# Performance work log

Measured on AMD Instinct MI355X. Metric: run time of the kernel, lower is better.

The kernel has to match this reference:

```python
import jax, jax.numpy as jnp
import numpy as np

NUM_HEADS = 4
NUM_GROUPS = 8
EPS = 1e-5


def group_norm(x, gamma, beta):
    # x: [b, c, h, w], GroupNorm with NUM_GROUPS groups, eps=1e-5
    b, c, h, w = x.shape
    xg = x.reshape(b, NUM_GROUPS, (c // NUM_GROUPS) * h * w)
    mean = jnp.mean(xg, axis=-1, keepdims=True)
    var = jnp.var(xg, axis=-1, keepdims=True)
    xn = ((xg - mean) * jax.lax.rsqrt(var + EPS)).reshape(b, c, h, w)
    return xn * gamma[None, :, None, None] + beta[None, :, None, None]


def setup_inputs() -> dict:
    key = jax.random.key(0)
    ks = jax.random.split(key, 4)
    b, c, h, w = 4, 256, 64, 64
    x = jax.random.normal(ks[0], (b, c, h, w), dtype=jnp.float32)
    gamma = jnp.ones((c,), dtype=jnp.float32)
    beta = jnp.zeros((c,), dtype=jnp.float32)
    w_qkv = jax.random.normal(ks[1], (3 * c, c), dtype=jnp.float32) * (c ** -0.5)
    b_qkv = jnp.zeros((3 * c,), dtype=jnp.float32)
    w_proj = jax.random.normal(ks[2], (c, c), dtype=jnp.float32) * (c ** -0.5)
    b_proj = jnp.zeros((c,), dtype=jnp.float32)
    return {"x": x, "gamma": gamma, "beta": beta, "w_qkv": w_qkv,
            "b_qkv": b_qkv, "w_proj": w_proj, "b_proj": b_proj}


def reference(x, gamma, beta, w_qkv, b_qkv, w_proj, b_proj):
    b, c, h, w = x.shape
    heads = NUM_HEADS
    dim = c // heads
    n = h * w
    residual = x
    xn = group_norm(x, gamma, beta)
    # 1x1 conv == per-pixel linear: [b,c,h,w] x [3c,c] -> [b,3c,h,w]
    qkv = jnp.einsum('bchw,oc->bohw', xn, w_qkv) + b_qkv[None, :, None, None]
    # channel layout: (three, heads, dim)
    qkv = qkv.reshape(b, 3, heads, dim, n)            # [b,3,H,D,N]
    qkv = jnp.transpose(qkv, (1, 0, 2, 4, 3))         # [3,b,H,N,D]
    q, k, v = qkv[0], qkv[1], qkv[2]
    scale = dim ** -0.5
    scores = jnp.einsum('bhid,bhjd->bhij', q * scale, k)  # [b,H,N,N]
    attn = jax.nn.softmax(scores, axis=-1)
    out = jnp.einsum('bhij,bhjd->bhid', attn, v)          # [b,H,N,D]
    out = jnp.transpose(out, (0, 1, 3, 2)).reshape(b, c, h, w)
    out = jnp.einsum('bchw,oc->bohw', out, w_proj) + b_proj[None, :, None, None]
    return out + residual
```

## Files before the change

kernel.cpp:

```cpp
#include <hip/hip_runtime.h>
#include <stdint.h>

typedef unsigned short ushort_t;
typedef __attribute__((ext_vector_type(8))) short bf16x8;
typedef __attribute__((ext_vector_type(4))) float f32x4;
typedef __attribute__((ext_vector_type(16))) float f32x16;
typedef __attribute__((ext_vector_type(4))) unsigned int u32x4;

__device__ __forceinline__ ushort_t f2bf(float f) {
  union { float f; unsigned u; } v; v.f = f;
  unsigned r = v.u + 0x7fffu + ((v.u >> 16) & 1u);
  return (ushort_t)(r >> 16);
}
__device__ __forceinline__ unsigned bfbits(float f) {
  union { float f; unsigned u; } v; v.f = f; return v.u;
}
__device__ __forceinline__ unsigned pack_trunc(float lo, float hi) {
#if __has_builtin(__builtin_amdgcn_perm)
  return __builtin_amdgcn_perm(bfbits(hi), bfbits(lo), 0x07060302u);
#else
  return (bfbits(lo) >> 16) | (bfbits(hi) & 0xffff0000u);
#endif
}
__device__ __forceinline__ unsigned pack_rn(float lo, float hi) {
  return (unsigned)f2bf(lo) | ((unsigned)f2bf(hi) << 16);
}
__device__ __forceinline__ void swap32(unsigned &a, unsigned &b) {
#if __has_builtin(__builtin_amdgcn_permlane32_swap)
  auto r = __builtin_amdgcn_permlane32_swap(a, b, false, false);
  a = r[0]; b = r[1];
#else
  asm volatile("v_permlane32_swap_b32 %0, %1" : "+v"(a), "+v"(b));
#endif
}
__device__ __forceinline__ float fast_exp2(float x) {
#if __has_builtin(__builtin_amdgcn_exp2f)
  return __builtin_amdgcn_exp2f(x);
#else
  float r; asm("v_exp_f32 %0, %1" : "=v"(r) : "v"(x)); return r;
#endif
}

#define SCALE_Q 0.18033688011112042f
#define EXP_BIAS 23.083109273961734f

__global__ __launch_bounds__(256)
void gn_stats1(const float* __restrict__ x, float2* __restrict__ partial) {
  int blk = blockIdx.x, tid = threadIdx.x;
  const float* base = x + (size_t)blk * 16384;
  float s = 0.f, ss = 0.f;
  for (int i = tid * 4; i < 16384; i += 1024) {
    float4 v = *(const float4*)(base + i);
    s  += v.x + v.y + v.z + v.w;
    ss += v.x*v.x + v.y*v.y + v.z*v.z + v.w*v.w;
  }
  __shared__ float rs[256], rss[256];
  rs[tid] = s; rss[tid] = ss;
  __syncthreads();
  for (int off = 128; off > 0; off >>= 1) {
    if (tid < off) { rs[tid] += rs[tid+off]; rss[tid] += rss[tid+off]; }
    __syncthreads();
  }
  if (tid == 0) partial[blk] = make_float2(rs[0], rss[0]);
}

__global__ __launch_bounds__(256)
void gn_apply_t(const float* __restrict__ x, const float2* __restrict__ partial,
                const float* __restrict__ gamma, const float* __restrict__ beta,
                ushort_t* __restrict__ xn_t, int b0) {
  int blk = blockIdx.x;
  int tid = threadIdx.x;
  int ct = blk & 7;
  int nt = (blk >> 3) & 15;
  int bl = blk >> 7;
  int b  = b0 + bl;
  int c0 = ct * 32;
  float s = 0.f, ss = 0.f;
  #pragma unroll
  for (int kk = 0; kk < 8; kk++) {
    float2 p = partial[(b*8 + ct)*8 + kk];
    s += p.x; ss += p.y;
  }
  float mean = s * (1.f/131072.f);
  float rstd = rsqrtf(ss * (1.f/131072.f) - mean*mean + 1e-5f);
  __shared__ ushort_t Ls[32][264];
  for (int idx = tid; idx < 32*64; idx += 256) {
    int cc = idx >> 6, seg = idx & 63;
    float ga = gamma[c0+cc], be = beta[c0+cc];
    float a = rstd * ga;
    float bb = be - mean * a;
    float4 v = *(const float4*)(x + ((size_t)(b*256 + c0 + cc))*4096 + nt*256 + seg*4);
    ushort4 t4 = make_ushort4(f2bf(v.x*a+bb), f2bf(v.y*a+bb), f2bf(v.z*a+bb), f2bf(v.w*a+bb));
    *(ushort4*)&Ls[cc][seg*4] = t4;
  }
  __syncthreads();
  for (int idx = tid; idx < 256*4; idx += 256) {
    int n = idx >> 2, seg = idx & 3;
    union { ushort_t u[8]; uint4 v; } pk;
    #pragma unroll
    for (int e = 0; e < 8; e++) pk.u[e] = Ls[seg*8 + e][n];
    *(uint4*)(xn_t + ((size_t)(bl*4096 + nt*256 + n))*256 + c0 + seg*8) = pk.v;
  }
}

__global__ __launch_bounds__(256)
void wconv2(const float* __restrict__ wq, const float* __restrict__ wp,
            ushort_t* __restrict__ oq, ushort_t* __restrict__ op) {
  int blk = blockIdx.x;
  const float* w; ushort_t* o; int i;
  if (blk < 192) { w = wq; o = oq; i = blk*256 + threadIdx.x; }
  else           { w = wp; o = op; i = (blk-192)*256 + threadIdx.x; }
  float4 v = *(const float4*)(w + (size_t)i*4);
  *(ushort4*)(o + (size_t)i*4) = make_ushort4(f2bf(v.x), f2bf(v.y), f2bf(v.z), f2bf(v.w));
}

__global__ __launch_bounds__(256)
void gemm_qkv(const ushort_t* __restrict__ A, const ushort_t* __restrict__ Bt,
              const float* __restrict__ bias, ushort_t* __restrict__ q,
              ushort_t* __restrict__ kbuf, ushort_t* __restrict__ vt,
              int b0, int cpx) {
  int L = blockIdx.x;
  int blk = (L & 7) * cpx + (L >> 3);
  int nt = blk % 12, mt = blk / 12;
  int m0 = mt*128, n0 = nt*64;
  int tid = threadIdx.x;
  int wave = tid >> 6, lane = tid & 63, quad = lane >> 4, l16 = lane & 15;
  __shared__ ushort_t As[128][40];
  __shared__ ushort_t Bs[64][40];
  __shared__ ushort_t Lt[64][136];
  f32x4 acc[2][4];
  #pragma unroll
  for (int i = 0; i < 2; i++)
    #pragma unroll
    for (int j = 0; j < 4; j++) acc[i][j] = (f32x4){0.f,0.f,0.f,0.f};

  for (int k0 = 0; k0 < 256; k0 += 32) {
    #pragma unroll
    for (int i = tid; i < 512; i += 256) {
      int row = i >> 2, seg = i & 3;
      *(uint4*)&As[row][seg*8] = *(const uint4*)(A + (size_t)(m0+row)*256 + k0 + seg*8);
    }
    {
      int row = tid >> 2, seg = tid & 3;
      *(uint4*)&Bs[row][seg*8] = *(const uint4*)(Bt + (size_t)(n0+row)*256 + k0 + seg*8);
    }
    __syncthreads();
    bf16x8 af[2], bfr[4];
    #pragma unroll
    for (int t = 0; t < 2; t++) af[t]  = *(const bf16x8*)&As[wave*32 + t*16 + l16][quad*8];
    #pragma unroll
    for (int t = 0; t < 4; t++) bfr[t] = *(const bf16x8*)&Bs[t*16 + l16][quad*8];
    #pragma unroll
    for (int ti = 0; ti < 2; ti++)
      #pragma unroll
      for (int jn = 0; jn < 4; jn++)
        acc[ti][jn] = __builtin_amdgcn_mfma_f32_16x16x32_bf16(af[ti], bfr[jn], acc[ti][jn], 0, 0, 0);
    __syncthreads();
  }

  int region = nt >> 2;
  if (region == 0) {
    #pragma unroll
    for (int jn = 0; jn < 4; jn++) {
      int n = n0 + jn*16 + l16;
      float bv = bias[n];
      #pragma unroll
      for (int ti = 0; ti < 2; ti++) {
        int mrow = m0 + wave*32 + ti*16 + quad*4;
        #pragma unroll
        for (int r = 0; r < 4; r++)
          q[(size_t)(b0*4096 + mrow + r)*256 + n] = f2bf((acc[ti][jn][r] + bv) * SCALE_Q);
      }
    }
  } else if (region == 1) {
    #pragma unroll
    for (int jn = 0; jn < 4; jn++) {
      int n = n0 + jn*16 + l16;
      float bv = bias[n];
      #pragma unroll
      for (int ti = 0; ti < 2; ti++) {
        int mrow = m0 + wave*32 + ti*16 + quad*4;
        #pragma unroll
        for (int r = 0; r < 4; r++)
          kbuf[(size_t)(b0*4096 + mrow + r)*256 + (n - 256)] = f2bf(acc[ti][jn][r] + bv);
      }
    }
  } else {
    int hh = nt - 8;
    int b_loc = m0 >> 12;
    #pragma unroll
    for (int jn = 0; jn < 4; jn++) {
      int n = n0 + jn*16 + l16;
      float bv = bias[n];
      int drow = jn*16 + l16;
      #pragma unroll
      for (int ti = 0; ti < 2; ti++) {
        int tcol = wave*32 + ti*16 + quad*4;
        uint2 w;
        w.x = pack_rn(acc[ti][jn][0] + bv, acc[ti][jn][1] + bv);
        w.y = pack_rn(acc[ti][jn][2] + bv, acc[ti][jn][3] + bv);
        *(uint2*)&Lt[drow][tcol] = w;
      }
    }
    __syncthreads();
    size_t vb_ = ((size_t)((b0 + b_loc)*4 + hh)*64)*4096 + (size_t)(m0 & 4095);
    for (int idx = tid; idx < 1024; idx += 256) {
      int dd = idx >> 4, toff = (idx & 15)*8;
      *(uint4*)(vt + vb_ + (size_t)dd*4096 + toff) = *(const uint4*)&Lt[dd][toff];
    }
  }
}

__global__ __launch_bounds__(256)
void attn(ushort_t* __restrict__ q, const ushort_t* __restrict__ k,
          const ushort_t* __restrict__ vt, int cpx) {
  int L = blockIdx.x;
  int blk = (L & 7) * cpx + (L >> 3);
  int it = blk & 31;
  int h  = (blk >> 5) & 3;
  int b  = blk >> 7;
  int i0 = it * 128;
  int tid = threadIdx.x;
  int wave = tid >> 6, lane = tid & 63;
  int q32 = lane & 31, hi = lane >> 5;

  __shared__ ushort_t Ks[2][64][72];
  __shared__ ushort_t Vs[2][64][72];

  const ushort_t* kbase = k + (size_t)(b*4096)*256 + h*64;
  const ushort_t* vbase = vt + (size_t)(b*4 + h)*64*4096;
  ushort_t* qrow = q + (size_t)(b*4096 + i0 + wave*32 + q32)*256 + h*64;

  bf16x8 qb0 = *(const bf16x8*)(qrow      + hi*8);
  bf16x8 qb1 = *(const bf16x8*)(qrow + 16 + hi*8);
  bf16x8 qb2 = *(const bf16x8*)(qrow + 32 + hi*8);
  bf16x8 qb3 = *(const bf16x8*)(qrow + 48 + hi*8);

  bf16x8 ones;
  #pragma unroll
  for (int e = 0; e < 8; e++) ones[e] = (short)0x3F80;

  f32x16 bias_init;
  #pragma unroll
  for (int r = 0; r < 16; r++) bias_init[r] = -EXP_BIAS;

  f32x16 o_acc0, o_acc1, l_acc;
  #pragma unroll
  for (int r = 0; r < 16; r++) { o_acc0[r] = 0.f; o_acc1[r] = 0.f; l_acc[r] = 0.f; }

  int srow = tid >> 2, scol = (tid & 3) * 16;
  const ushort_t* kp = kbase + (size_t)srow*256 + scol;
  const ushort_t* vp = vbase + (size_t)srow*4096 + scol;
  uint4 rk0, rk1, rv0, rv1;
  #define LOADK() { \
    rk0 = *(const uint4*)(kp); \
    rk1 = *(const uint4*)(kp + 8); \
    kp += 64*256; }
  #define WRITEK(BI) { \
    *(uint4*)&Ks[BI][srow][scol]     = rk0; \
    *(uint4*)&Ks[BI][srow][scol + 8] = rk1; }
  #define LOADV() { \
    rv0 = *(const uint4*)(vp); \
    rv1 = *(const uint4*)(vp + 8); \
    vp += 64; }
  #define WRITEV(BI) { \
    *(uint4*)&Vs[BI][srow][scol]     = rv0; \
    *(uint4*)&Vs[BI][srow][scol + 8] = rv1; }

  #define SOFTMAX(S, PB0, PB1) \
    _Pragma("unroll") \
    for (int r = 0; r < 16; r++) S[r] = fast_exp2(S[r]); \
    { unsigned pkA = pack_trunc(S[0],  S[1]),  pkB = pack_trunc(S[2],  S[3]); \
      unsigned pkC = pack_trunc(S[4],  S[5]),  pkD = pack_trunc(S[6],  S[7]); \
      unsigned pkE = pack_trunc(S[8],  S[9]),  pkF = pack_trunc(S[10], S[11]); \
      unsigned pkG = pack_trunc(S[12], S[13]), pkH = pack_trunc(S[14], S[15]); \
      swap32(pkA, pkC); swap32(pkB, pkD); \
      swap32(pkE, pkG); swap32(pkF, pkH); \
      u32x4 w0_ = {pkA, pkB, pkC, pkD}; \
      u32x4 w1_ = {pkE, pkF, pkG, pkH}; \
      PB0 = __builtin_bit_cast(bf16x8, w0_); \
      PB1 = __builtin_bit_cast(bf16x8, w1_); }

  #define WINDOW(BI) { \
    bf16x8 k00 = *(const bf16x8*)&Ks[BI][q32     ][hi*8]; \
    bf16x8 k01 = *(const bf16x8*)&Ks[BI][q32     ][16 + hi*8]; \
    bf16x8 k02 = *(const bf16x8*)&Ks[BI][q32     ][32 + hi*8]; \
    bf16x8 k03 = *(const bf16x8*)&Ks[BI][q32     ][48 + hi*8]; \
    bf16x8 k10 = *(const bf16x8*)&Ks[BI][32 + q32][hi*8]; \
    bf16x8 k11 = *(const bf16x8*)&Ks[BI][32 + q32][16 + hi*8]; \
    bf16x8 k12 = *(const bf16x8*)&Ks[BI][32 + q32][32 + hi*8]; \
    bf16x8 k13 = *(const bf16x8*)&Ks[BI][32 + q32][48 + hi*8]; \
    bf16x8 va00 = *(const bf16x8*)&Vs[BI][q32     ][hi*8]; \
    bf16x8 va01 = *(const bf16x8*)&Vs[BI][q32     ][16 + hi*8]; \
    bf16x8 va10 = *(const bf16x8*)&Vs[BI][32 + q32][hi*8]; \
    bf16x8 va11 = *(const bf16x8*)&Vs[BI][32 + q32][16 + hi*8]; \
    __builtin_amdgcn_s_setprio(1); \
    f32x16 s0 = __builtin_amdgcn_mfma_f32_32x32x16_bf16(k00, qb0, bias_init, 0, 0, 0); \
    s0 = __builtin_amdgcn_mfma_f32_32x32x16_bf16(k01, qb1, s0, 0, 0, 0); \
    s0 = __builtin_amdgcn_mfma_f32_32x32x16_bf16(k02, qb2, s0, 0, 0, 0); \
    s0 = __builtin_amdgcn_mfma_f32_32x32x16_bf16(k03, qb3, s0, 0, 0, 0); \
    f32x16 s1 = __builtin_amdgcn_mfma_f32_32x32x16_bf16(k10, qb0, bias_init, 0, 0, 0); \
    s1 = __builtin_amdgcn_mfma_f32_32x32x16_bf16(k11, qb1, s1, 0, 0, 0); \
    s1 = __builtin_amdgcn_mfma_f32_32x32x16_bf16(k12, qb2, s1, 0, 0, 0); \
    s1 = __builtin_amdgcn_mfma_f32_32x32x16_bf16(k13, qb3, s1, 0, 0, 0); \
    __builtin_amdgcn_s_setprio(0); \
    bf16x8 vc00 = *(const bf16x8*)&Vs[BI][q32     ][32 + hi*8]; \
    bf16x8 vc01 = *(const bf16x8*)&Vs[BI][q32     ][48 + hi*8]; \
    bf16x8 vc10 = *(const bf16x8*)&Vs[BI][32 + q32][32 + hi*8]; \
    bf16x8 vc11 = *(const bf16x8*)&Vs[BI][32 + q32][48 + hi*8]; \
    bf16x8 pb00, pb01, pb10, pb11; \
    SOFTMAX(s0, pb00, pb01)    \
    __builtin_amdgcn_s_setprio(1); \
    o_acc0 = __builtin_amdgcn_mfma_f32_32x32x16_bf16(va00, pb00, o_acc0, 0, 0, 0); \
    o_acc0 = __builtin_amdgcn_mfma_f32_32x32x16_bf16(va01, pb01, o_acc0, 0, 0, 0); \
    o_acc1 = __builtin_amdgcn_mfma_f32_32x32x16_bf16(va10, pb00, o_acc1, 0, 0, 0); \
    o_acc1 = __builtin_amdgcn_mfma_f32_32x32x16_bf16(va11, pb01, o_acc1, 0, 0, 0); \
    l_acc  = __builtin_amdgcn_mfma_f32_32x32x16_bf16(ones, pb00, l_acc, 0, 0, 0); \
    l_acc  = __builtin_amdgcn_mfma_f32_32x32x16_bf16(ones, pb01, l_acc, 0, 0, 0); \
    __builtin_amdgcn_s_setprio(0); \
    SOFTMAX(s1, pb10, pb11)    \
    __builtin_amdgcn_s_setprio(1); \
    o_acc0 = __builtin_amdgcn_mfma_f32_32x32x16_bf16(vc00, pb10, o_acc0, 0, 0, 0); \
    o_acc0 = __builtin_amdgcn_mfma_f32_32x32x16_bf16(vc01, pb11, o_acc0, 0, 0, 0); \
    o_acc1 = __builtin_amdgcn_mfma_f32_32x32x16_bf16(vc10, pb10, o_acc1, 0, 0, 0); \
    o_acc1 = __builtin_amdgcn_mfma_f32_32x32x16_bf16(vc11, pb11, o_acc1, 0, 0, 0); \
    l_acc  = __builtin_amdgcn_mfma_f32_32x32x16_bf16(ones, pb10, l_acc, 0, 0, 0); \
    l_acc  = __builtin_amdgcn_mfma_f32_32x32x16_bf16(ones, pb11, l_acc, 0, 0, 0); \
    __builtin_amdgcn_s_setprio(0); \
  }

  LOADK(); LOADV(); WRITEK(0); WRITEV(0);
  __syncthreads();

  #pragma unroll 2
  for (int w = 0; w < 64; w++) {
    int cur = w & 1;
    if (w < 63) { LOADK(); LOADV(); }
    WINDOW(cur)
    if (w < 63) { WRITEK(cur ^ 1); WRITEV(cur ^ 1); }
    __syncthreads();
  }
  #undef LOADK
  #undef LOADV
  #undef WRITEK
  #undef WRITEV
  #undef WINDOW
  #undef SOFTMAX

  float inv = 1.f / l_acc[0];

  #pragma unroll
  for (int g = 0; g < 4; g++) {
    ushort4 u;
    u.x = f2bf(o_acc0[g*4+0]*inv); u.y = f2bf(o_acc0[g*4+1]*inv);
    u.z = f2bf(o_acc0[g*4+2]*inv); u.w = f2bf(o_acc0[g*4+3]*inv);
    *(ushort4*)(qrow + g*8 + hi*4) = u;
  }
  #pragma unroll
  for (int g = 0; g < 4; g++) {
    ushort4 u;
    u.x = f2bf(o_acc1[g*4+0]*inv); u.y = f2bf(o_acc1[g*4+1]*inv);
    u.z = f2bf(o_acc1[g*4+2]*inv); u.w = f2bf(o_acc1[g*4+3]*inv);
    *(ushort4*)(qrow + 32 + g*8 + hi*4) = u;
  }
}

__global__ __launch_bounds__(256)
void gemm_proj(const ushort_t* __restrict__ A,
               const ushort_t* __restrict__ Bt,
               const float* __restrict__ bias, const float* __restrict__ resid,
               float* __restrict__ out, int col_base) {
  int blk = blockIdx.x;
  int mt = blk & 1, nt = blk >> 1;
  int m0 = mt*128, n0 = nt*64;
  int tid = threadIdx.x;
  int wave = tid >> 6, lane = tid & 63, quad = lane >> 4, l16 = lane & 15;
  __shared__ ushort_t As[128][40];
  __shared__ ushort_t Bs[64][40];
  f32x4 acc[2][4];
  #pragma unroll
  for (int i = 0; i < 2; i++)
    #pragma unroll
    for (int j = 0; j < 4; j++) acc[i][j] = (f32x4){0.f,0.f,0.f,0.f};

  for (int k0 = 0; k0 < 256; k0 += 32) {
    #pragma unroll
    for (int i = tid; i < 512; i += 256) {
      int row = i >> 2, seg = i & 3;
      *(uint4*)&As[row][seg*8] = *(const uint4*)(A + (size_t)(m0+row)*256 + k0 + seg*8);
    }
    {
      int row = tid >> 2, seg = tid & 3;
      *(uint4*)&Bs[row][seg*8] = *(const uint4*)(Bt + (size_t)(n0+row)*256 + k0 + seg*8);
    }
    __syncthreads();
    bf16x8 af[2], bfr[4];
    #pragma unroll
    for (int t = 0; t < 2; t++) af[t]  = *(const bf16x8*)&As[wave*32 + t*16 + l16][quad*8];
    #pragma unroll
    for (int t = 0; t < 4; t++) bfr[t] = *(const bf16x8*)&Bs[t*16 + l16][quad*8];
    #pragma unroll
    for (int ti = 0; ti < 2; ti++)
      #pragma unroll
      for (int jn = 0; jn < 4; jn++)
        acc[ti][jn] = __builtin_amdgcn_mfma_f32_16x16x32_bf16(af[ti], bfr[jn], acc[ti][jn], 0, 0, 0);
    __syncthreads();
  }
  #pragma unroll
  for (int jn = 0; jn < 4; jn++) {
    int col = col_base + n0 + jn*16 + l16;
    int bb = col >> 12;
    int np = col & 4095;
    #pragma unroll
    for (int ti = 0; ti < 2; ti++) {
      int o = m0 + wave*32 + ti*16 + quad*4;
      #pragma unroll
      for (int r = 0; r < 4; r++) {
        int oo = o + r;
        size_t addr = ((size_t)(bb*256 + oo))*4096 + np;
        out[addr] = acc[ti][jn][r] + bias[oo] + resid[addr];
      }
    }
  }
}

extern "C" void kernel_launch(void* const* d_in, const int* in_sizes, int n_in,
                              void* d_out, int out_size, void* d_ws, size_t ws_size,
                              hipStream_t stream) {
  const float* x      = (const float*)d_in[0];
  const float* gamma  = (const float*)d_in[1];
  const float* beta   = (const float*)d_in[2];
  const float* w_qkv  = (const float*)d_in[3];
  const float* b_qkv  = (const float*)d_in[4];
  const float* w_proj = (const float*)d_in[5];
  const float* b_proj = (const float*)d_in[6];
  float* out = (float*)d_out;

  char* ws = (char*)d_ws;
  float2* partial  = (float2*)(ws + 1024);
  ushort_t* wqkv_bf  = (ushort_t*)(ws + 4096);
  ushort_t* wproj_bf = (ushort_t*)(ws + 397312);
  char* big = ws + 528384;

  gn_stats1<<<dim3(256), dim3(256), 0, stream>>>(x, partial);
  wconv2<<<dim3(256), dim3(256), 0, stream>>>(w_qkv, w_proj, wqkv_bf, wproj_bf);

  if (ws_size >= (size_t)528384 + 3*(size_t)8388608 + (size_t)4194304) {
    ushort_t* q    = (ushort_t*)big;
    ushort_t* kbuf = (ushort_t*)(big + (size_t)8388608);
    ushort_t* vt   = (ushort_t*)(big + (size_t)16777216);
    ushort_t* xn   = (ushort_t*)(big + (size_t)25165824);
    for (int c = 0; c < 2; c++) {
      int b0 = c * 2;
      gn_apply_t<<<dim3(256), dim3(256), 0, stream>>>(x, partial, gamma, beta, xn, b0);
      gemm_qkv<<<dim3(768), dim3(256), 0, stream>>>(xn, wqkv_bf, b_qkv, q, kbuf, vt, b0, 96);
    }
    attn<<<dim3(512), dim3(256), 0, stream>>>(q, kbuf, vt, 64);
    gemm_proj<<<dim3(512), dim3(256), 0, stream>>>(wproj_bf, q, b_proj, x, out, 0);
  } else {
    ushort_t* q_c  = (ushort_t*)big;
    ushort_t* k_c  = (ushort_t*)(big + (size_t)2097152);
    ushort_t* vt_c = (ushort_t*)(big + (size_t)4194304);
    ushort_t* xn_c = (ushort_t*)(big + (size_t)6291456);
    for (int b0 = 0; b0 < 4; b0++) {
      gn_apply_t<<<dim3(128), dim3(256), 0, stream>>>(x, partial, gamma, beta, xn_c, b0);
      gemm_qkv<<<dim3(384), dim3(256), 0, stream>>>(xn_c, wqkv_bf, b_qkv, q_c, k_c, vt_c, 0, 48);
      attn<<<dim3(128), dim3(256), 0, stream>>>(q_c, k_c, vt_c, 16);
      gemm_proj<<<dim3(128), dim3(256), 0, stream>>>(wproj_bf, q_c, b_proj, x, out, b0*4096);
    }
  }
}
```

Baseline: 222.1 us.

## Double attention KV window to 128 keys and software-pipeline QK/softmax/PV

Each loop iteration of the attention kernel now stages 128 keys of K and V into LDS instead of 64. This halves the number of __syncthreads barriers and loop iterations. Within a window, the QK, softmax and PV steps for four 32-key sub-blocks are interleaved so that the next QK MFMAs can overlap the exp/pack work of the previous sub-block. The cost is double the LDS (about 73KB) and more live registers (four score tiles plus double global prefetch registers), which may reduce occupancy.

```diff
diff --git a/kernel.cpp b/kernel.cpp
--- a/kernel.cpp
+++ b/kernel.cpp
@@ -224,8 +224,8 @@
   int wave = tid >> 6, lane = tid & 63;
   int q32 = lane & 31, hi = lane >> 5;
 
-  __shared__ ushort_t Ks[2][64][72];
-  __shared__ ushort_t Vs[2][64][72];
+  __shared__ ushort_t Ks[2][128][72];
+  __shared__ ushort_t Vs[2][64][136];
 
   const ushort_t* kbase = k + (size_t)(b*4096)*256 + h*64;
   const ushort_t* vbase = vt + (size_t)(b*4 + h)*64*4096;
@@ -248,24 +248,37 @@
   #pragma unroll
   for (int r = 0; r < 16; r++) { o_acc0[r] = 0.f; o_acc1[r] = 0.f; l_acc[r] = 0.f; }
 
-  int srow = tid >> 2, scol = (tid & 3) * 16;
-  const ushort_t* kp = kbase + (size_t)srow*256 + scol;
-  const ushort_t* vp = vbase + (size_t)srow*4096 + scol;
-  uint4 rk0, rk1, rv0, rv1;
+  int kr = tid >> 1, kc = (tid & 1) * 32;
+  int vr = tid >> 2, vc = (tid & 3) * 32;
+  const ushort_t* kp = kbase + (size_t)kr*256 + kc;
+  const ushort_t* vp = vbase + (size_t)vr*4096 + vc;
+  uint4 rk0, rk1, rk2, rk3, rv0, rv1, rv2, rv3;
   #define LOADK() { \
-    rk0 = *(const uint4*)(kp); \
-    rk1 = *(const uint4*)(kp + 8); \
-    kp += 64*256; }
+    rk0 = *(const uint4*)(kp);      rk1 = *(const uint4*)(kp + 8); \
+    rk2 = *(const uint4*)(kp + 16); rk3 = *(const uint4*)(kp + 24); \
+    kp += 128*256; }
   #define WRITEK(BI) { \
-    *(uint4*)&Ks[BI][srow][scol]     = rk0; \
-    *(uint4*)&Ks[BI][srow][scol + 8] = rk1; }
+    *(uint4*)&Ks[BI][kr][kc]      = rk0; *(uint4*)&Ks[BI][kr][kc + 8]  = rk1; \
+    *(uint4*)&Ks[BI][kr][kc + 16] = rk2; *(uint4*)&Ks[BI][kr][kc + 24] = rk3; }
   #define LOADV() { \
-    rv0 = *(const uint4*)(vp); \
-    rv1 = *(const uint4*)(vp + 8); \
-    vp += 64; }
+    rv0 = *(const uint4*)(vp);      rv1 = *(const uint4*)(vp + 8); \
+    rv2 = *(const uint4*)(vp + 16); rv3 = *(const uint4*)(vp + 24); \
+    vp += 128; }
   #define WRITEV(BI) { \
-    *(uint4*)&Vs[BI][srow][scol]     = rv0; \
-    *(uint4*)&Vs[BI][srow][scol + 8] = rv1; }
+    *(uint4*)&Vs[BI][vr][vc]      = rv0; *(uint4*)&Vs[BI][vr][vc + 8]  = rv1; \
+    *(uint4*)&Vs[BI][vr][vc + 16] = rv2; *(uint4*)&Vs[BI][vr][vc + 24] = rv3; }
+
+  #define QK(BI, SS, SV) { \
+    bf16x8 ka = *(const bf16x8*)&Ks[BI][(SS)*32 + q32][hi*8]; \
+    bf16x8 kb = *(const bf16x8*)&Ks[BI][(SS)*32 + q32][16 + hi*8]; \
+    bf16x8 kc = *(const bf16x8*)&Ks[BI][(SS)*32 + q32][32 + hi*8]; \
+    bf16x8 kd = *(const bf16x8*)&Ks[BI][(SS)*32 + q32][48 + hi*8]; \
+    __builtin_amdgcn_s_setprio(1); \
+    SV = __builtin_amdgcn_mfma_f32_32x32x16_bf16(ka, qb0, bias_init, 0, 0, 0); \
+    SV = __builtin_amdgcn_mfma_f32_32x32x16_bf16(kb, qb1, SV, 0, 0, 0); \
+    SV = __builtin_amdgcn_mfma_f32_32x32x16_bf16(kc, qb2, SV, 0, 0, 0); \
+    SV = __builtin_amdgcn_mfma_f32_32x32x16_bf16(kd, qb3, SV, 0, 0, 0); \
+    __builtin_amdgcn_s_setprio(0); }
 
   #define SOFTMAX(S, PB0, PB1) \
     _Pragma("unroll") \
@@ -281,63 +294,46 @@
       PB0 = __builtin_bit_cast(bf16x8, w0_); \
       PB1 = __builtin_bit_cast(bf16x8, w1_); }
 
+  #define PV(BI, SS, PB0, PB1) { \
+    bf16x8 va = *(const bf16x8*)&Vs[BI][q32     ][(SS)*32 + hi*8]; \
+    bf16x8 vb = *(const bf16x8*)&Vs[BI][q32     ][(SS)*32 + 16 + hi*8]; \
+    bf16x8 vc_ = *(const bf16x8*)&Vs[BI][32 + q32][(SS)*32 + hi*8]; \
+    bf16x8 vd = *(const bf16x8*)&Vs[BI][32 + q32][(SS)*32 + 16 + hi*8]; \
+    __builtin_amdgcn_s_setprio(1); \
+    o_acc0 = __builtin_amdgcn_mfma_f32_32x32x16_bf16(va, PB0, o_acc0, 0, 0, 0); \
+    o_acc0 = __builtin_amdgcn_mfma_f32_32x32x16_bf16(vb, PB1, o_acc0, 0, 0, 0); \
+    o_acc1 = __builtin_amdgcn_mfma_f32_32x32x16_bf16(vc_, PB0, o_acc1, 0, 0, 0); \
+    o_acc1 = __builtin_amdgcn_mfma_f32_32x32x16_bf16(vd, PB1, o_acc1, 0, 0, 0); \
+    l_acc  = __builtin_amdgcn_mfma_f32_32x32x16_bf16(ones, PB0, l_acc, 0, 0, 0); \
+    l_acc  = __builtin_amdgcn_mfma_f32_32x32x16_bf16(ones, PB1, l_acc, 0, 0, 0); \
+    __builtin_amdgcn_s_setprio(0); }
+
   #define WINDOW(BI) { \
-    bf16x8 k00 = *(const bf16x8*)&Ks[BI][q32     ][hi*8]; \
-    bf16x8 k01 = *(const bf16x8*)&Ks[BI][q32     ][16 + hi*8]; \
-    bf16x8 k02 = *(const bf16x8*)&Ks[BI][q32     ][32 + hi*8]; \
-    bf16x8 k03 = *(const bf16x8*)&Ks[BI][q32     ][48 + hi*8]; \
-    bf16x8 k10 = *(const bf16x8*)&Ks[BI][32 + q32][hi*8]; \
-    bf16x8 k11 = *(const bf16x8*)&Ks[BI][32 + q32][16 + hi*8]; \
-    bf16x8 k12 = *(const bf16x8*)&Ks[BI][32 + q32][32 + hi*8]; \
-    bf16x8 k13 = *(const bf16x8*)&Ks[BI][32 + q32][48 + hi*8]; \
-    bf16x8 va00 = *(const bf16x8*)&Vs[BI][q32     ][hi*8]; \
-    bf16x8 va01 = *(const bf16x8*)&Vs[BI][q32     ][16 + hi*8]; \
-    bf16x8 va10 = *(const bf16x8*)&Vs[BI][32 + q32][hi*8]; \
-    bf16x8 va11 = *(const bf16x8*)&Vs[BI][32 + q32][16 + hi*8]; \
-    __builtin_amdgcn_s_setprio(1); \
-    f32x16 s0 = __builtin_amdgcn_mfma_f32_32x32x16_bf16(k00, qb0, bias_init, 0, 0, 0); \
-    s0 = __builtin_amdgcn_mfma_f32_32x32x16_bf16(k01, qb1, s0, 0, 0, 0); \
-    s0 = __builtin_amdgcn_mfma_f32_32x32x16_bf16(k02, qb2, s0, 0, 0, 0); \
-    s0 = __builtin_amdgcn_mfma_f32_32x32x16_bf16(k03, qb3, s0, 0, 0, 0); \
-    f32x16 s1 = __builtin_amdgcn_mfma_f32_32x32x16_bf16(k10, qb0, bias_init, 0, 0, 0); \
-    s1 = __builtin_amdgcn_mfma_f32_32x32x16_bf16(k11, qb1, s1, 0, 0, 0); \
-    s1 = __builtin_amdgcn_mfma_f32_32x32x16_bf16(k12, qb2, s1, 0, 0, 0); \
-    s1 = __builtin_amdgcn_mfma_f32_32x32x16_bf16(k13, qb3, s1, 0, 0, 0); \
-    __builtin_amdgcn_s_setprio(0); \
-    bf16x8 vc00 = *(const bf16x8*)&Vs[BI][q32     ][32 + hi*8]; \
-    bf16x8 vc01 = *(const bf16x8*)&Vs[BI][q32     ][48 + hi*8]; \
-    bf16x8 vc10 = *(const bf16x8*)&Vs[BI][32 + q32][32 + hi*8]; \
-    bf16x8 vc11 = *(const bf16x8*)&Vs[BI][32 + q32][48 + hi*8]; \
-    bf16x8 pb00, pb01, pb10, pb11; \
-    SOFTMAX(s0, pb00, pb01)    \
-    __builtin_amdgcn_s_setprio(1); \
-    o_acc0 = __builtin_amdgcn_mfma_f32_32x32x16_bf16(va00, pb00, o_acc0, 0, 0, 0); \
-    o_acc0 = __builtin_amdgcn_mfma_f32_32x32x16_bf16(va01, pb01, o_acc0, 0, 0, 0); \
-    o_acc1 = __builtin_amdgcn_mfma_f32_32x32x16_bf16(va10, pb00, o_acc1, 0, 0, 0); \
-    o_acc1 = __builtin_amdgcn_mfma_f32_32x32x16_bf16(va11, pb01, o_acc1, 0, 0, 0); \
-    l_acc  = __builtin_amdgcn_mfma_f32_32x32x16_bf16(ones, pb00, l_acc, 0, 0, 0); \
-    l_acc  = __builtin_amdgcn_mfma_f32_32x32x16_bf16(ones, pb01, l_acc, 0, 0, 0); \
-    __builtin_amdgcn_s_setprio(0); \
-    SOFTMAX(s1, pb10, pb11)    \
-    __builtin_amdgcn_s_setprio(1); \
-    o_acc0 = __builtin_amdgcn_mfma_f32_32x32x16_bf16(vc00, pb10, o_acc0, 0, 0, 0); \
-    o_acc0 = __builtin_amdgcn_mfma_f32_32x32x16_bf16(vc01, pb11, o_acc0, 0, 0, 0); \
-    o_acc1 = __builtin_amdgcn_mfma_f32_32x32x16_bf16(vc10, pb10, o_acc1, 0, 0, 0); \
-    o_acc1 = __builtin_amdgcn_mfma_f32_32x32x16_bf16(vc11, pb11, o_acc1, 0, 0, 0); \
-    l_acc  = __builtin_amdgcn_mfma_f32_32x32x16_bf16(ones, pb10, l_acc, 0, 0, 0); \
-    l_acc  = __builtin_amdgcn_mfma_f32_32x32x16_bf16(ones, pb11, l_acc, 0, 0, 0); \
-    __builtin_amdgcn_s_setprio(0); \
+    f32x16 s0, s1, s2, s3; \
+    bf16x8 p00, p01, p10, p11, p20, p21, p30, p31; \
+    QK(BI, 0, s0) \
+    QK(BI, 1, s1) \
+    SOFTMAX(s0, p00, p01) \
+    QK(BI, 2, s2) \
+    PV(BI, 0, p00, p01) \
+    SOFTMAX(s1, p10, p11) \
+    QK(BI, 3, s3) \
+    PV(BI, 1, p10, p11) \
+    SOFTMAX(s2, p20, p21) \
+    PV(BI, 2, p20, p21) \
+    SOFTMAX(s3, p30, p31) \
+    PV(BI, 3, p30, p31) \
   }
 
   LOADK(); LOADV(); WRITEK(0); WRITEV(0);
   __syncthreads();
 
   #pragma unroll 2
-  for (int w = 0; w < 64; w++) {
+  for (int w = 0; w < 32; w++) {
     int cur = w & 1;
-    if (w < 63) { LOADK(); LOADV(); }
+    if (w < 31) { LOADK(); LOADV(); }
     WINDOW(cur)
-    if (w < 63) { WRITEK(cur ^ 1); WRITEV(cur ^ 1); }
+    if (w < 31) { WRITEK(cur ^ 1); WRITEV(cur ^ 1); }
     __syncthreads();
   }
   #undef LOADK
@@ -345,6 +341,8 @@
   #undef WRITEK
   #undef WRITEV
   #undef WINDOW
+  #undef QK
+  #undef PV
   #undef SOFTMAX
 
   float inv = 1.f / l_acc[0];
```

New measurement: 222.7 us. About the same (+0.3%).
